# Kernel tuning notes

Measured on AMD Instinct MI355X. Metric: run time of the kernel, lower is better.

## Reference

```python
import jax, jax.numpy as jnp
import numpy as np

S, B, I, H = 512, 8192, 3, 5  # seq, batch, input_size, hidden_size


def _uniform(key, shape, bound):
    return jax.random.uniform(key, shape, jnp.float32, -bound, bound)


def setup_inputs() -> dict:
    key = jax.random.key(0)
    ks = jax.random.split(key, 17)
    bound = 1.0 / np.sqrt(H)
    inp = {"x": jax.random.normal(ks[0], (S, B, I), jnp.float32)}
    # layer 0: in=I ; layer 1: in=2H (concat of both directions). Suffix 'r' = reverse direction.
    specs = [
        ("l0", I), ("l0r", I), ("l1", 2 * H), ("l1r", 2 * H),
    ]
    ki = 1
    for name, din in specs:
        inp[f"w_ih_{name}"] = _uniform(ks[ki], (4 * H, din), bound); ki += 1
        inp[f"w_hh_{name}"] = _uniform(ks[ki], (4 * H, H), bound); ki += 1
        inp[f"b_ih_{name}"] = _uniform(ks[ki], (4 * H,), bound); ki += 1
        inp[f"b_hh_{name}"] = _uniform(ks[ki], (4 * H,), bound); ki += 1
    return inp


def _lstm_dir(x, w_ih, w_hh, b_ih, b_hh, reverse):
    """Single-direction LSTM over x [S,B,Din] -> (hs [S,B,H], h_T [B,H], c_T [B,H])."""
    xs = x[::-1] if reverse else x
    # Precompute input contributions for all timesteps in one big matmul.
    gx = jnp.einsum('sbi,gi->sbg', xs, w_ih) + b_ih + b_hh  # [S,B,4H]
    h0 = jnp.zeros((x.shape[1], H), x.dtype)
    c0 = jnp.zeros((x.shape[1], H), x.dtype)

    def step(carry, g):
        h, c = carry
        g = g + h @ w_hh.T  # [B,4H]
        i, f, gg, o = jnp.split(g, 4, axis=-1)  # PyTorch gate order: i,f,g,o
        i = jax.nn.sigmoid(i)
        f = jax.nn.sigmoid(f)
        gg = jnp.tanh(gg)
        o = jax.nn.sigmoid(o)
        c = f * c + i * gg
        h = o * jnp.tanh(c)
        return (h, c), h

    (hT, cT), hs = jax.lax.scan(step, (h0, c0), gx)
    if reverse:
        hs = hs[::-1]
    return hs, hT, cT


def reference(x,
              w_ih_l0, w_hh_l0, b_ih_l0, b_hh_l0,
              w_ih_l0r, w_hh_l0r, b_ih_l0r, b_hh_l0r,
              w_ih_l1, w_hh_l1, b_ih_l1, b_hh_l1,
              w_ih_l1r, w_hh_l1r, b_ih_l1r, b_hh_l1r):
    # Layer 0 (bidirectional)
    hs0f, h0f, c0f = _lstm_dir(x, w_ih_l0, w_hh_l0, b_ih_l0, b_hh_l0, False)
    hs0b, h0b, c0b = _lstm_dir(x, w_ih_l0r, w_hh_l0r, b_ih_l0r, b_hh_l0r, True)
    out0 = jnp.concatenate([hs0f, hs0b], axis=-1)  # [S,B,2H]
    # Layer 1 (bidirectional) consumes concat of both directions
    hs1f, h1f, c1f = _lstm_dir(out0, w_ih_l1, w_hh_l1, b_ih_l1, b_hh_l1, False)
    hs1b, h1b, c1b = _lstm_dir(out0, w_ih_l1r, w_hh_l1r, b_ih_l1r, b_hh_l1r, True)
    output = jnp.concatenate([hs1f, hs1b], axis=-1)  # [S,B,2H]
    # PyTorch h_n/c_n layout: [num_layers*num_directions, B, H] ordered (l0 fwd, l0 bwd, l1 fwd, l1 bwd)
    h_n = jnp.stack([h0f, h0b, h1f, h1b], axis=0)
    c_n = jnp.stack([c0f, c0b, c1f, c1b], axis=0)
    return output, h_n, c_n
```

## Files before the change

### kernel.cpp

```cpp
#include <hip/hip_runtime.h>


constexpr int S_ = 512;
constexpr int B_ = 8192;
constexpr int NROW = 16384;

constexpr int GD1  = 1366;
constexpr int TL   = 208;
constexpr int GSTR = GD1 * 64;

constexpr float L2E  = 1.4426950408889634f;
constexpr float T2E  = 2.8853900817779268f;
constexpr float IT2E = 0.34657359027997264f;

typedef _Float16 v2h __attribute__((ext_vector_type(2)));

__device__ __forceinline__ float dot2h(v2h a, v2h b, float c) {
#if __has_builtin(__builtin_amdgcn_fdot2)
    return __builtin_amdgcn_fdot2(a, b, c, false);
#else
    return fmaf((float)a[0], (float)b[0], fmaf((float)a[1], (float)b[1], c));
#endif
}

__device__ __forceinline__ float rcp_(float x) { return __builtin_amdgcn_rcpf(x); }

__device__ __forceinline__ float exp2_(float x) {
#if __has_builtin(__builtin_amdgcn_exp2f)
    return __builtin_amdgcn_exp2f(x);
#else
    return exp2f(x);
#endif
}

__device__ __forceinline__ void sbar() { __builtin_amdgcn_sched_barrier(0); }

__device__ __forceinline__ float bperm(int bidx, float v) {
    return __int_as_float(__builtin_amdgcn_ds_bpermute(bidx, __float_as_int(v)));
}

__device__ __forceinline__ unsigned pkh(float a, float b) {
    auto t = __builtin_amdgcn_cvt_pkrtz(a, b);
    unsigned q; __builtin_memcpy(&q, &t, 4); return q;
}

__device__ __forceinline__ unsigned short f2h(float x) {
    _Float16 h = (_Float16)x;
    unsigned short s; __builtin_memcpy(&s, &h, 2); return s;
}

__device__ __forceinline__ float h2f(unsigned short s) {
    _Float16 h; __builtin_memcpy(&h, &s, 2); return (float)h;
}

__device__ __forceinline__ int xswz1366(int bid) {
    const int xcd = bid & 7, loc = bid >> 3;
    const int base = (xcd < 6) ? xcd * 171 : 1026 + (xcd - 6) * 170;
    return base + loc;
}

__global__ __launch_bounds__(64) __attribute__((amdgpu_waves_per_eu(1, 2)))
void lstm_layer0(
    const float* __restrict__ x,
    const float* __restrict__ wih_f, const float* __restrict__ whh_f,
    const float* __restrict__ bih_f, const float* __restrict__ bhh_f,
    const float* __restrict__ wih_r, const float* __restrict__ whh_r,
    const float* __restrict__ bih_r, const float* __restrict__ bhh_r,
    unsigned short* __restrict__ ws,
    float* __restrict__ outbase)
{
    const int l64 = threadIdx.x & 63;
    int r = l64 / 5; r = (r > 11) ? 11 : r;
    const int u   = l64 - r * 5;
    const int uc  = (u < 5) ? u : 4;
    const int bsw = xswz1366((int)blockIdx.x);
    const int gid = bsw * 12 + r;
    const bool valid = gid < NROW;
    const int dir = (gid >> 13) & 1;
    const int b   = gid & 8191;
    const bool stw = valid && (u < 3);
    const bool st  = valid && (u < 5);

    int bidx[5];
#pragma unroll
    for (int k = 0; k < 5; k++) bidx[k] = (r * 5 + k) * 4;

    const float* __restrict__ wih = dir ? wih_r : wih_f;
    const float* __restrict__ whh = dir ? whh_r : whh_f;
    const float* __restrict__ bih = dir ? bih_r : bih_f;
    const float* __restrict__ bhh = dir ? bhh_r : bhh_f;

    const int rows[4] = {uc, 5 + uc, 10 + uc, 15 + uc};
    const float scl[4] = {-L2E, -L2E, T2E, -L2E};
    float WX[4][3], WH[4][5], BS[4];
#pragma unroll
    for (int gi = 0; gi < 4; gi++) {
        const int rr = rows[gi]; const float sc = scl[gi];
#pragma unroll
        for (int i = 0; i < 3; i++) WX[gi][i] = wih[rr * 3 + i] * sc;
#pragma unroll
        for (int k = 0; k < 5; k++) WH[gi][k] = whh[rr * 5 + k] * sc;
        BS[gi] = (bih[rr] + bhh[rr]) * sc;
    }

    float h[5] = {0.f, 0.f, 0.f, 0.f, 0.f};
    float cp = 0.f, hu_last = 0.f;

    const int t0 = dir ? (S_ - 1) : 0;
    const float* xp = x + ((size_t)t0 * B_ + b) * 3;
    unsigned short* wp = ws + (size_t)dir * ((size_t)S_ * B_ * 6)
                            + ((size_t)t0 * B_ + b) * 6;
    const ptrdiff_t xst = dir ? -(ptrdiff_t)3 * B_ : (ptrdiff_t)3 * B_;
    const ptrdiff_t wst = dir ? -(ptrdiff_t)6 * B_ : (ptrdiff_t)6 * B_;

    auto step = [&](const float (&xin)[3], unsigned short* wpp) {
        float a0 = BS[0], a1 = BS[1], a2 = BS[2], a3 = BS[3];
#pragma unroll
        for (int i = 0; i < 3; i++) {
            a0 = fmaf(WX[0][i], xin[i], a0);
            a1 = fmaf(WX[1][i], xin[i], a1);
            a2 = fmaf(WX[2][i], xin[i], a2);
            a3 = fmaf(WX[3][i], xin[i], a3);
        }
#pragma unroll
        for (int k = 0; k < 5; k++) {
            a0 = fmaf(WH[0][k], h[k], a0);
            a1 = fmaf(WH[1][k], h[k], a1);
            a2 = fmaf(WH[2][k], h[k], a2);
            a3 = fmaf(WH[3][k], h[k], a3);
        }
        const float ig = rcp_(1.0f + exp2_(a0));
        const float fg = rcp_(1.0f + exp2_(a1));
        const float g2 = fmaf(-2.0f * T2E, rcp_(1.0f + exp2_(a2)), T2E);
        const float og = rcp_(1.0f + exp2_(a3));
        cp = fmaf(fg, cp, ig * g2);
        const float th = fmaf(-2.0f, rcp_(1.0f + exp2_(cp)), 1.0f);
        const float hu = og * th;
        hu_last = hu;
#pragma unroll
        for (int k = 0; k < 5; k++) h[k] = bperm(bidx[k], hu);
        const unsigned q0 = pkh(h[0], h[1]);
        const unsigned q1 = pkh(h[2], h[3]);
        const unsigned q2 = pkh(h[4], 0.0f);
        unsigned qs = q0;
        qs = (u == 1) ? q1 : qs;
        qs = (u == 2) ? q2 : qs;
        if (stw) ((unsigned*)wpp)[u] = qs;
    };

    auto ld = [&](float (&buf)[3]) {
        __builtin_memcpy(&buf[0], xp, 12);
        xp += xst;
        sbar();
    };

    float x0[3], x1[3], x2[3], x3[3], x4[3], x5[3], x6[3], x7[3];
    ld(x0); ld(x1); ld(x2); ld(x3); ld(x4); ld(x5); ld(x6); ld(x7);

#pragma unroll 1
    for (int s = 0; s < S_ - 8; s += 8) {
        step(x0, wp); wp += wst; ld(x0);
        step(x1, wp); wp += wst; ld(x1);
        step(x2, wp); wp += wst; ld(x2);
        step(x3, wp); wp += wst; ld(x3);
        step(x4, wp); wp += wst; ld(x4);
        step(x5, wp); wp += wst; ld(x5);
        step(x6, wp); wp += wst; ld(x6);
        step(x7, wp); wp += wst; ld(x7);
    }
    step(x0, wp); wp += wst;
    step(x1, wp); wp += wst;
    step(x2, wp); wp += wst;
    step(x3, wp); wp += wst;
    step(x4, wp); wp += wst;
    step(x5, wp); wp += wst;
    step(x6, wp); wp += wst;
    step(x7, wp);

    const size_t OUTE = (size_t)S_ * B_ * 10;
    float* hn = outbase + OUTE + ((size_t)dir * B_ + b) * 5;
    float* cn = hn + (size_t)4 * B_ * 5;
    if (st) { hn[uc] = hu_last; cn[uc] = cp * IT2E; }
}

__global__ __launch_bounds__(64) __attribute__((amdgpu_waves_per_eu(1, 2)))
void lstm_layer1(
    const unsigned short* __restrict__ ws,
    const float* __restrict__ wih_f, const float* __restrict__ whh_f,
    const float* __restrict__ bih_f, const float* __restrict__ bhh_f,
    const float* __restrict__ wih_r, const float* __restrict__ whh_r,
    const float* __restrict__ bih_r, const float* __restrict__ bhh_r,
    float* __restrict__ outbase,
    unsigned short* __restrict__ gtemp)
{
    __shared__ unsigned short lt[TL * 60];

    const int l64 = threadIdx.x & 63;
    const int bid = (int)blockIdx.x;
    const int bsw = xswz1366(bid);
    int r = l64 / 5; r = (r > 11) ? 11 : r;
    const int u   = l64 - r * 5;
    const int uc  = (u < 5) ? u : 4;
    const int rm  = (r < 6) ? r : r - 6;
    const int dir = (r >= 6) ? 1 : 0;
    const int braw = bsw * 6 + rm;
    const bool valid = braw < B_;
    const int b   = valid ? braw : (B_ - 1);
    const bool st = valid && (u < 5);
    const bool lw = (l64 < 60);
    const int dir5 = dir * 5;
    const int pr  = dir ? (r - 6) : (r + 6);
    const int ps  = pr * 5 + uc;

    int bidx[5];
#pragma unroll
    for (int k = 0; k < 5; k++) bidx[k] = (r * 5 + k) * 4;

    const float* __restrict__ wih = dir ? wih_r : wih_f;
    const float* __restrict__ whh = dir ? whh_r : whh_f;
    const float* __restrict__ bih = dir ? bih_r : bih_f;
    const float* __restrict__ bhh = dir ? bhh_r : bhh_f;

    const int rows[4] = {uc, 5 + uc, 10 + uc, 15 + uc};
    const float scl[4] = {-L2E, -L2E, T2E, -L2E};
    v2h WX[4][6];
    float WH[4][5], BS[4];
#pragma unroll
    for (int gi = 0; gi < 4; gi++) {
        const int rr = rows[gi]; const float sc = scl[gi];
#pragma unroll
        for (int p = 0; p < 6; p++) {
            const int i0 = (p < 3) ? 2 * p : 2 * p - 1;
            const bool pad = (p == 2) || (p == 5);
            const float w0 = wih[rr * 10 + i0] * sc;
            const float w1 = pad ? 0.f : wih[rr * 10 + i0 + 1] * sc;
            WX[gi][p] = (v2h){(_Float16)w0, (_Float16)w1};
        }
#pragma unroll
        for (int k = 0; k < 5; k++) WH[gi][k] = whh[rr * 5 + k] * sc;
        BS[gi] = (bih[rr] + bhh[rr]) * sc;
    }

    float h[5] = {0.f, 0.f, 0.f, 0.f, 0.f};
    float cp = 0.f, hu_last = 0.f;

    const int t0 = dir ? (S_ - 1) : 0;
    const unsigned short* rpf = ws + ((size_t)t0 * B_ + b) * 6;
    const unsigned short* rpb = rpf + (size_t)S_ * B_ * 6;
    float* op = outbase + ((size_t)(dir ? 255 : 256) * B_ + b) * 10;
    const ptrdiff_t rst = dir ? -(ptrdiff_t)6 * B_ : (ptrdiff_t)6 * B_;
    const ptrdiff_t ost = dir ? -(ptrdiff_t)10 * B_ : (ptrdiff_t)10 * B_;

    unsigned short* gw = gtemp + (size_t)bid * 64 + l64;

    struct A4 { float a0, a1, a2, a3; };

    auto dots = [&](const v2h (&xin)[6]) -> A4 {
        A4 v;
        v.a0 = BS[0]; v.a1 = BS[1]; v.a2 = BS[2]; v.a3 = BS[3];
#pragma unroll
        for (int p = 0; p < 6; p++) {
            v.a0 = dot2h(xin[p], WX[0][p], v.a0);
            v.a1 = dot2h(xin[p], WX[1][p], v.a1);
            v.a2 = dot2h(xin[p], WX[2][p], v.a2);
            v.a3 = dot2h(xin[p], WX[3][p], v.a3);
        }
        return v;
    };

    auto cell = [&](A4 v) -> float {
#pragma unroll
        for (int k = 0; k < 5; k++) {
            v.a0 = fmaf(WH[0][k], h[k], v.a0);
            v.a1 = fmaf(WH[1][k], h[k], v.a1);
            v.a2 = fmaf(WH[2][k], h[k], v.a2);
            v.a3 = fmaf(WH[3][k], h[k], v.a3);
        }
        const float ig = rcp_(1.0f + exp2_(v.a0));
        const float fg = rcp_(1.0f + exp2_(v.a1));
        const float g2 = fmaf(-2.0f * T2E, rcp_(1.0f + exp2_(v.a2)), T2E);
        const float og = rcp_(1.0f + exp2_(v.a3));
        cp = fmaf(fg, cp, ig * g2);
        const float th = fmaf(-2.0f, rcp_(1.0f + exp2_(cp)), 1.0f);
        const float hu = og * th;
        hu_last = hu;
        return hu;
    };

    auto bcast = [&](float hu) {
#pragma unroll
        for (int k = 0; k < 5; k++) h[k] = bperm(bidx[k], hu);
    };

    auto ld = [&](v2h (&buf)[6]) {
        __builtin_memcpy(&buf[0], rpf, 12);
        __builtin_memcpy(&buf[3], rpb, 12);
        rpf += rst; rpb += rst;
        sbar();
    };

    auto s1L = [&](v2h (&xb)[6], int t) {
        A4 a = dots(xb); ld(xb);
        const float hu = cell(a); bcast(hu);
        if (lw) lt[t * 60 + l64] = f2h(hu);
    };
    auto s1G = [&](v2h (&xb)[6]) {
        A4 a = dots(xb); ld(xb);
        const float hu = cell(a); bcast(hu);
        *gw = f2h(hu); gw += GSTR;
    };
    auto s2G = [&](v2h (&xb)[6], unsigned short pvs) {
        A4 a = dots(xb); ld(xb);
        const float pv = h2f(pvs);
        const float hu = cell(a); bcast(hu);
        if (st) { op[dir5 + uc] = hu; op[5 - dir5 + uc] = pv; }
        op += ost;
    };
    auto s2L = [&](v2h (&xb)[6], int t) {
        const float pv = h2f(lt[(511 - t) * 60 + ps]);
        A4 a = dots(xb); ld(xb);
        const float hu = cell(a); bcast(hu);
        if (st) { op[dir5 + uc] = hu; op[5 - dir5 + uc] = pv; }
        op += ost;
    };
    auto s2Ln = [&](v2h (&xb)[6], int t) {
        const float pv = h2f(lt[(511 - t) * 60 + ps]);
        A4 a = dots(xb);
        const float hu = cell(a); bcast(hu);
        if (st) { op[dir5 + uc] = hu; op[5 - dir5 + uc] = pv; }
        op += ost;
    };

    v2h x0[6], x1[6], x2[6], x3[6], x4[6], x5[6], x6[6], x7[6];
    ld(x0); ld(x1); ld(x2); ld(x3); ld(x4); ld(x5); ld(x6); ld(x7);

#pragma unroll 1
    for (int t = 0; t < TL; t += 8) {
        s1L(x0, t + 0); s1L(x1, t + 1); s1L(x2, t + 2); s1L(x3, t + 3);
        s1L(x4, t + 4); s1L(x5, t + 5); s1L(x6, t + 6); s1L(x7, t + 7);
    }
#pragma unroll 1
    for (int t = TL; t < 256; t += 8) {
        s1G(x0); s1G(x1); s1G(x2); s1G(x3);
        s1G(x4); s1G(x5); s1G(x6); s1G(x7);
    }
    asm volatile("s_waitcnt vmcnt(0)" ::: "memory");
    const unsigned short* gb = gtemp + (size_t)bid * 64 + ps;
    unsigned short q0 = gb[(size_t)47 * GSTR];
    unsigned short q1 = gb[(size_t)46 * GSTR];
    unsigned short q2 = gb[(size_t)45 * GSTR];
    unsigned short q3 = gb[(size_t)44 * GSTR];
    const unsigned short* grq = gb + (size_t)43 * GSTR;
#pragma unroll 1
    for (int t = 256; t < 304; t += 8) {
        s2G(x0, q0); q0 = *grq; grq -= GSTR;
        s2G(x1, q1); q1 = *grq; grq -= GSTR;
        s2G(x2, q2); q2 = *grq; grq -= GSTR;
        s2G(x3, q3); q3 = *grq; grq -= GSTR;
        s2G(x4, q0); q0 = *grq; grq -= GSTR;
        s2G(x5, q1); q1 = *grq; grq -= GSTR;
        s2G(x6, q2); q2 = *grq; grq -= GSTR;
        s2G(x7, q3); q3 = *grq; grq -= GSTR;
    }
#pragma unroll 1
    for (int t = 304; t < 504; t += 8) {
        s2L(x0, t + 0); s2L(x1, t + 1); s2L(x2, t + 2); s2L(x3, t + 3);
        s2L(x4, t + 4); s2L(x5, t + 5); s2L(x6, t + 6); s2L(x7, t + 7);
    }
    s2Ln(x0, 504); s2Ln(x1, 505); s2Ln(x2, 506); s2Ln(x3, 507);
    s2Ln(x4, 508); s2Ln(x5, 509); s2Ln(x6, 510); s2Ln(x7, 511);

    const size_t OUTE = (size_t)S_ * B_ * 10;
    float* hn = outbase + OUTE + ((size_t)(2 + dir) * B_ + b) * 5;
    float* cn = hn + (size_t)4 * B_ * 5;
    if (st) { hn[uc] = hu_last; cn[uc] = cp * IT2E; }
}

extern "C" void kernel_launch(void* const* d_in, const int* in_sizes, int n_in,
                              void* d_out, int out_size, void* d_ws, size_t ws_size,
                              hipStream_t stream) {
    const float* x       = (const float*)d_in[0];
    const float* wih_l0  = (const float*)d_in[1];
    const float* whh_l0  = (const float*)d_in[2];
    const float* bih_l0  = (const float*)d_in[3];
    const float* bhh_l0  = (const float*)d_in[4];
    const float* wih_l0r = (const float*)d_in[5];
    const float* whh_l0r = (const float*)d_in[6];
    const float* bih_l0r = (const float*)d_in[7];
    const float* bhh_l0r = (const float*)d_in[8];
    const float* wih_l1  = (const float*)d_in[9];
    const float* whh_l1  = (const float*)d_in[10];
    const float* bih_l1  = (const float*)d_in[11];
    const float* bhh_l1  = (const float*)d_in[12];
    const float* wih_l1r = (const float*)d_in[13];
    const float* whh_l1r = (const float*)d_in[14];
    const float* bih_l1r = (const float*)d_in[15];
    const float* bhh_l1r = (const float*)d_in[16];

    float* out = (float*)d_out;
    unsigned short* ws = (unsigned short*)d_ws;
    unsigned short* gtemp = ws + (size_t)2 * S_ * B_ * 6 + (size_t)4 * GSTR;

    dim3 grid0(1366), block(64);
    lstm_layer0<<<grid0, block, 0, stream>>>(x,
        wih_l0, whh_l0, bih_l0, bhh_l0,
        wih_l0r, whh_l0r, bih_l0r, bhh_l0r,
        ws, out);
    dim3 grid1(GD1);
    lstm_layer1<<<grid1, block, 0, stream>>>(ws,
        wih_l1, whh_l1, bih_l1, bhh_l1,
        wih_l1r, whh_l1r, bih_l1r, bhh_l1r,
        out, gtemp);
}
```

Before: 310.7 us.

## Pack layer-0 hidden states into 16-byte groups of four timesteps

Layer 0 now buffers four timesteps of fp16 hidden output in registers and writes them as one 16-byte store into a grouped workspace layout (128 groups, 48 bytes per batch row). Layer 1 reads 48-byte chunks per direction plane and extracts each timestep's inputs with a direction-dependent index, replacing per-step 12-byte loads. The goal is fewer, wider memory transactions on the workspace traffic between layers. In exchange, layer 1 holds more prefetch registers, and the XCD block swizzle in layer 0 is removed, which may change L2 locality.

Result: slower. 319.5 us (+2.8%).

```diff
diff --git a/kernel.cpp b/kernel.cpp
--- a/kernel.cpp
+++ b/kernel.cpp
@@ -14,6 +14,7 @@
 constexpr float IT2E = 0.34657359027997264f;
 
 typedef _Float16 v2h __attribute__((ext_vector_type(2)));
+typedef unsigned u32;
 
 __device__ __forceinline__ float dot2h(v2h a, v2h b, float c) {
 #if __has_builtin(__builtin_amdgcn_fdot2)
@@ -58,6 +59,9 @@
     const int base = (xcd < 6) ? xcd * 171 : 1026 + (xcd - 6) * 170;
     return base + loc;
 }
+
+constexpr int GRP = 128;
+constexpr ptrdiff_t PLANE_DW = (ptrdiff_t)GRP * B_ * 12;
 
 __global__ __launch_bounds__(64) __attribute__((amdgpu_waves_per_eu(1, 2)))
 void lstm_layer0(
@@ -73,8 +77,7 @@
     int r = l64 / 5; r = (r > 11) ? 11 : r;
     const int u   = l64 - r * 5;
     const int uc  = (u < 5) ? u : 4;
-    const int bsw = xswz1366((int)blockIdx.x);
-    const int gid = bsw * 12 + r;
+    const int gid = blockIdx.x * 12 + r;
     const bool valid = gid < NROW;
     const int dir = (gid >> 13) & 1;
     const int b   = gid & 8191;
@@ -108,12 +111,14 @@
 
     const int t0 = dir ? (S_ - 1) : 0;
     const float* xp = x + ((size_t)t0 * B_ + b) * 3;
-    unsigned short* wp = ws + (size_t)dir * ((size_t)S_ * B_ * 6)
-                            + ((size_t)t0 * B_ + b) * 6;
     const ptrdiff_t xst = dir ? -(ptrdiff_t)3 * B_ : (ptrdiff_t)3 * B_;
-    const ptrdiff_t wst = dir ? -(ptrdiff_t)6 * B_ : (ptrdiff_t)6 * B_;
-
-    auto step = [&](const float (&xin)[3], unsigned short* wpp) {
+    u32* wp = (u32*)ws + (size_t)dir * PLANE_DW
+                       + ((size_t)(dir ? GRP - 1 : 0) * B_ + b) * 12 + u * 4;
+    const ptrdiff_t wst4 = dir ? -(ptrdiff_t)B_ * 12 : (ptrdiff_t)B_ * 12;
+
+    u32 acc[4];
+
+    auto step = [&](const float (&xin)[3], int slot) {
         float a0 = BS[0], a1 = BS[1], a2 = BS[2], a3 = BS[3];
 #pragma unroll
         for (int i = 0; i < 3; i++) {
@@ -145,7 +150,12 @@
         unsigned qs = q0;
         qs = (u == 1) ? q1 : qs;
         qs = (u == 2) ? q2 : qs;
-        if (stw) ((unsigned*)wpp)[u] = qs;
+        acc[slot] = qs;
+    };
+
+    auto flush = [&]() {
+        if (stw) __builtin_memcpy(__builtin_assume_aligned(wp, 16), acc, 16);
+        wp += wst4;
     };
 
     auto ld = [&](float (&buf)[3]) {
@@ -159,23 +169,23 @@
 
 #pragma unroll 1
     for (int s = 0; s < S_ - 8; s += 8) {
-        step(x0, wp); wp += wst; ld(x0);
-        step(x1, wp); wp += wst; ld(x1);
-        step(x2, wp); wp += wst; ld(x2);
-        step(x3, wp); wp += wst; ld(x3);
-        step(x4, wp); wp += wst; ld(x4);
-        step(x5, wp); wp += wst; ld(x5);
-        step(x6, wp); wp += wst; ld(x6);
-        step(x7, wp); wp += wst; ld(x7);
-    }
-    step(x0, wp); wp += wst;
-    step(x1, wp); wp += wst;
-    step(x2, wp); wp += wst;
-    step(x3, wp); wp += wst;
-    step(x4, wp); wp += wst;
-    step(x5, wp); wp += wst;
-    step(x6, wp); wp += wst;
-    step(x7, wp);
+        step(x0, 0); ld(x0);
+        step(x1, 1); ld(x1);
+        step(x2, 2); ld(x2);
+        step(x3, 3); ld(x3); flush();
+        step(x4, 0); ld(x4);
+        step(x5, 1); ld(x5);
+        step(x6, 2); ld(x6);
+        step(x7, 3); ld(x7); flush();
+    }
+    step(x0, 0);
+    step(x1, 1);
+    step(x2, 2);
+    step(x3, 3); flush();
+    step(x4, 0);
+    step(x5, 1);
+    step(x6, 2);
+    step(x7, 3); flush();
 
     const size_t OUTE = (size_t)S_ * B_ * 10;
     float* hn = outbase + OUTE + ((size_t)dir * B_ + b) * 5;
@@ -244,11 +254,13 @@
     float h[5] = {0.f, 0.f, 0.f, 0.f, 0.f};
     float cp = 0.f, hu_last = 0.f;
 
-    const int t0 = dir ? (S_ - 1) : 0;
-    const unsigned short* rpf = ws + ((size_t)t0 * B_ + b) * 6;
-    const unsigned short* rpb = rpf + (size_t)S_ * B_ * 6;
+    const u32* wsd = (const u32*)ws;
+    const int g0 = dir ? (GRP - 1) : 0;
+    const u32* rp0 = wsd + ((size_t)g0 * B_ + b) * 12;
+    const u32* rp1 = wsd + PLANE_DW + ((size_t)g0 * B_ + b) * 12;
+    const ptrdiff_t gst = dir ? -(ptrdiff_t)B_ * 12 : (ptrdiff_t)B_ * 12;
+
     float* op = outbase + ((size_t)(dir ? 255 : 256) * B_ + b) * 10;
-    const ptrdiff_t rst = dir ? -(ptrdiff_t)6 * B_ : (ptrdiff_t)6 * B_;
     const ptrdiff_t ost = dir ? -(ptrdiff_t)10 * B_ : (ptrdiff_t)10 * B_;
 
     unsigned short* gw = gtemp + (size_t)bid * 64 + l64;
@@ -292,57 +304,79 @@
         for (int k = 0; k < 5; k++) h[k] = bperm(bidx[k], hu);
     };
 
-    auto ld = [&](v2h (&buf)[6]) {
-        __builtin_memcpy(&buf[0], rpf, 12);
-        __builtin_memcpy(&buf[3], rpb, 12);
-        rpf += rst; rpb += rst;
+    u32 A0[12], A1[12], B0[12], B1[12];
+    v2h xt[6];
+
+    auto ldg = [&](u32 (&P0)[12], u32 (&P1)[12]) {
+        __builtin_memcpy(P0, __builtin_assume_aligned(rp0, 16), 48);
+        __builtin_memcpy(P1, __builtin_assume_aligned(rp1, 16), 48);
+        rp0 += gst; rp1 += gst;
         sbar();
     };
 
-    auto s1L = [&](v2h (&xb)[6], int t) {
-        A4 a = dots(xb); ld(xb);
+    auto mkx = [&](const u32 (&P0)[12], const u32 (&P1)[12], int p) {
+#pragma unroll
+        for (int j = 0; j < 3; j++) {
+            const u32 a = dir ? P0[j * 4 + 3 - p] : P0[j * 4 + p];
+            const u32 c = dir ? P1[j * 4 + p]     : P1[j * 4 + 3 - p];
+            __builtin_memcpy(&xt[j], &a, 4);
+            __builtin_memcpy(&xt[3 + j], &c, 4);
+        }
+    };
+
+    auto s1L = [&](int t) {
+        A4 a = dots(xt);
         const float hu = cell(a); bcast(hu);
         if (lw) lt[t * 60 + l64] = f2h(hu);
     };
-    auto s1G = [&](v2h (&xb)[6]) {
-        A4 a = dots(xb); ld(xb);
+    auto s1G = [&]() {
+        A4 a = dots(xt);
         const float hu = cell(a); bcast(hu);
         *gw = f2h(hu); gw += GSTR;
     };
-    auto s2G = [&](v2h (&xb)[6], unsigned short pvs) {
-        A4 a = dots(xb); ld(xb);
+    auto s2G = [&](unsigned short pvs) {
+        A4 a = dots(xt);
         const float pv = h2f(pvs);
         const float hu = cell(a); bcast(hu);
         if (st) { op[dir5 + uc] = hu; op[5 - dir5 + uc] = pv; }
         op += ost;
     };
-    auto s2L = [&](v2h (&xb)[6], int t) {
+    auto s2L = [&](int t) {
         const float pv = h2f(lt[(511 - t) * 60 + ps]);
-        A4 a = dots(xb); ld(xb);
+        A4 a = dots(xt);
         const float hu = cell(a); bcast(hu);
         if (st) { op[dir5 + uc] = hu; op[5 - dir5 + uc] = pv; }
         op += ost;
     };
-    auto s2Ln = [&](v2h (&xb)[6], int t) {
-        const float pv = h2f(lt[(511 - t) * 60 + ps]);
-        A4 a = dots(xb);
-        const float hu = cell(a); bcast(hu);
-        if (st) { op[dir5 + uc] = hu; op[5 - dir5 + uc] = pv; }
-        op += ost;
-    };
-
-    v2h x0[6], x1[6], x2[6], x3[6], x4[6], x5[6], x6[6], x7[6];
-    ld(x0); ld(x1); ld(x2); ld(x3); ld(x4); ld(x5); ld(x6); ld(x7);
+
+    ldg(A0, A1);
+    ldg(B0, B1);
 
 #pragma unroll 1
     for (int t = 0; t < TL; t += 8) {
-        s1L(x0, t + 0); s1L(x1, t + 1); s1L(x2, t + 2); s1L(x3, t + 3);
-        s1L(x4, t + 4); s1L(x5, t + 5); s1L(x6, t + 6); s1L(x7, t + 7);
+        mkx(A0, A1, 0); s1L(t + 0);
+        mkx(A0, A1, 1); s1L(t + 1);
+        mkx(A0, A1, 2); s1L(t + 2);
+        mkx(A0, A1, 3); s1L(t + 3);
+        ldg(A0, A1);
+        mkx(B0, B1, 0); s1L(t + 4);
+        mkx(B0, B1, 1); s1L(t + 5);
+        mkx(B0, B1, 2); s1L(t + 6);
+        mkx(B0, B1, 3); s1L(t + 7);
+        ldg(B0, B1);
     }
 #pragma unroll 1
     for (int t = TL; t < 256; t += 8) {
-        s1G(x0); s1G(x1); s1G(x2); s1G(x3);
-        s1G(x4); s1G(x5); s1G(x6); s1G(x7);
+        mkx(A0, A1, 0); s1G();
+        mkx(A0, A1, 1); s1G();
+        mkx(A0, A1, 2); s1G();
+        mkx(A0, A1, 3); s1G();
+        ldg(A0, A1);
+        mkx(B0, B1, 0); s1G();
+        mkx(B0, B1, 1); s1G();
+        mkx(B0, B1, 2); s1G();
+        mkx(B0, B1, 3); s1G();
+        ldg(B0, B1);
     }
     asm volatile("s_waitcnt vmcnt(0)" ::: "memory");
     const unsigned short* gb = gtemp + (size_t)bid * 64 + ps;
@@ -353,22 +387,38 @@
     const unsigned short* grq = gb + (size_t)43 * GSTR;
 #pragma unroll 1
     for (int t = 256; t < 304; t += 8) {
-        s2G(x0, q0); q0 = *grq; grq -= GSTR;
-        s2G(x1, q1); q1 = *grq; grq -= GSTR;
-        s2G(x2, q2); q2 = *grq; grq -= GSTR;
-        s2G(x3, q3); q3 = *grq; grq -= GSTR;
-        s2G(x4, q0); q0 = *grq; grq -= GSTR;
-        s2G(x5, q1); q1 = *grq; grq -= GSTR;
-        s2G(x6, q2); q2 = *grq; grq -= GSTR;
-        s2G(x7, q3); q3 = *grq; grq -= GSTR;
+        mkx(A0, A1, 0); s2G(q0); q0 = *grq; grq -= GSTR;
+        mkx(A0, A1, 1); s2G(q1); q1 = *grq; grq -= GSTR;
+        mkx(A0, A1, 2); s2G(q2); q2 = *grq; grq -= GSTR;
+        mkx(A0, A1, 3); s2G(q3); q3 = *grq; grq -= GSTR;
+        ldg(A0, A1);
+        mkx(B0, B1, 0); s2G(q0); q0 = *grq; grq -= GSTR;
+        mkx(B0, B1, 1); s2G(q1); q1 = *grq; grq -= GSTR;
+        mkx(B0, B1, 2); s2G(q2); q2 = *grq; grq -= GSTR;
+        mkx(B0, B1, 3); s2G(q3); q3 = *grq; grq -= GSTR;
+        ldg(B0, B1);
     }
 #pragma unroll 1
     for (int t = 304; t < 504; t += 8) {
-        s2L(x0, t + 0); s2L(x1, t + 1); s2L(x2, t + 2); s2L(x3, t + 3);
-        s2L(x4, t + 4); s2L(x5, t + 5); s2L(x6, t + 6); s2L(x7, t + 7);
-    }
-    s2Ln(x0, 504); s2Ln(x1, 505); s2Ln(x2, 506); s2Ln(x3, 507);
-    s2Ln(x4, 508); s2Ln(x5, 509); s2Ln(x6, 510); s2Ln(x7, 511);
+        mkx(A0, A1, 0); s2L(t + 0);
+        mkx(A0, A1, 1); s2L(t + 1);
+        mkx(A0, A1, 2); s2L(t + 2);
+        mkx(A0, A1, 3); s2L(t + 3);
+        ldg(A0, A1);
+        mkx(B0, B1, 0); s2L(t + 4);
+        mkx(B0, B1, 1); s2L(t + 5);
+        mkx(B0, B1, 2); s2L(t + 6);
+        mkx(B0, B1, 3); s2L(t + 7);
+        ldg(B0, B1);
+    }
+    mkx(A0, A1, 0); s2L(504);
+    mkx(A0, A1, 1); s2L(505);
+    mkx(A0, A1, 2); s2L(506);
+    mkx(A0, A1, 3); s2L(507);
+    mkx(B0, B1, 0); s2L(508);
+    mkx(B0, B1, 1); s2L(509);
+    mkx(B0, B1, 2); s2L(510);
+    mkx(B0, B1, 3); s2L(511);
 
     const size_t OUTE = (size_t)S_ * B_ * 10;
     float* hn = outbase + OUTE + ((size_t)(2 + dir) * B_ + b) * 5;
```
